# Kernel tuning notes

Measured on AMD Instinct MI355X. Metric: run time of the kernel, lower is better.

The kernel has to match this reference:

```python
import jax, jax.numpy as jnp
import numpy as np

NEG = -1e9  # matches torch masked_fill value (additive, not -inf)

def setup_inputs() -> dict:
    key = jax.random.key(0)
    k1, k2, k3, k4 = jax.random.split(key, 4)
    B, H, S, D = 8, 16, 1024, 64
    q = jax.random.normal(k1, (B, H, S, D), dtype=jnp.float32)
    k = jax.random.normal(k2, (B, H, S, D), dtype=jnp.float32)
    v = jax.random.normal(k3, (B, H, S, D), dtype=jnp.float32)
    event_length = jax.random.randint(k4, (B,), 0, S, dtype=jnp.int32)
    return {"q": q, "k": k, "v": v, "event_length": event_length}

def reference(q, k, v, event_length):
    B, H, S, D = q.shape
    scale = 1.0 / jnp.sqrt(jnp.asarray(D, dtype=q.dtype))
    idx = jnp.arange(S)
    # valid[b, i] = i < event_length[b]
    valid = idx[None, :] < event_length[:, None]            # [B, S]
    # additive mask: 0 where (row valid AND col valid), else -1e9
    pair = valid[:, :, None] & valid[:, None, :]            # [B, S, S]
    attn_mask = jnp.where(pair, 0.0, NEG).astype(q.dtype)[:, None, :, :]  # [B,1,S,S]
    scores = jnp.einsum('bhqd,bhkd->bhqk', q, k) * scale + attn_mask
    probs = jax.nn.softmax(scores, axis=-1)
    out = jnp.einsum('bhqk,bhkd->bhqd', probs, v)
    return out
```

## Files before the change

### kernel.cpp

```cpp
#include <hip/hip_runtime.h>


#define Sdim 1024
#define Ddim 64
#define PITCH 72

typedef float f32x4 __attribute__((ext_vector_type(4)));
typedef _Float16 f16x8 __attribute__((ext_vector_type(8)));
typedef unsigned short u16x8 __attribute__((ext_vector_type(8)));
typedef unsigned int u32x2 __attribute__((ext_vector_type(2)));

union FragU { u16x8 u; f16x8 h; };

__device__ __forceinline__ unsigned pk2(float a, float b) {
  auto h = __builtin_amdgcn_cvt_pkrtz(a, b);
  return __builtin_bit_cast(unsigned, h);
}

__device__ __forceinline__ float fexp2(float x) {
  float r;
  asm("v_exp_f32 %0, %1" : "=v"(r) : "v"(x));
  return r;
}

__global__ __launch_bounds__(256, 3)
void attn_fwd(const float* __restrict__ Q, const float* __restrict__ K,
              const float* __restrict__ V, const int* __restrict__ EL,
              float* __restrict__ Out, unsigned* __restrict__ queues) {
  __shared__ unsigned short k_lds[64 * PITCH];
  __shared__ unsigned short v_lds[64 * PITCH];
  __shared__ unsigned short p_lds[4][32 * PITCH];
  __shared__ int s_item;

  const int tid   = threadIdx.x;
  const int homeq = blockIdx.x & 7;
  unsigned* ctr = &queues[homeq * 32];

  const int w    = tid >> 6;
  const int lane = tid & 63;
  const int r    = lane & 15;
  const int hi   = lane >> 4;
  const int r3   = r >> 3;
  const int sr   = tid >> 4;
  const int sc   = tid & 15;
  const int vskew = ((sc >> 1) & 7) * 8;

  for (;;) {
    __syncthreads();
    if (tid == 0) s_item = (int)atomicAdd(ctr, 1u);
    __syncthreads();
    const int g = s_item;
    if (g >= 128) break;

    const int pan = g >> 3;
    const int qt  = g & 7;
    const int bh  = pan * 8 + homeq;
    const int L   = EL[bh >> 4];

    const size_t base = (size_t)bh * Sdim * Ddim;
    const float* Qb = Q + base;
    const float* Kb = K + base;
    const float* Vb = V + base;
    float* ob = Out + base;

    const int q0blk = qt * 128;

    if (q0blk >= L) {
      float* red = (float*)k_lds;
      const int sc4 = sc * 4;
      const float* vp = Vb + (size_t)sr * Ddim + sc4;
      float4 acc = {0.f, 0.f, 0.f, 0.f};
#pragma unroll 8
      for (int i = 0; i < 64; ++i) {
        float4 a = *(const float4*)(vp + (size_t)i * 16 * Ddim);
        acc.x += a.x; acc.y += a.y; acc.z += a.z; acc.w += a.w;
      }
      *(float4*)&red[sr * 68 + sc4] = acc;
      __syncthreads();
      if (tid < 16) {
        float4 s = {0.f, 0.f, 0.f, 0.f};
#pragma unroll
        for (int i = 0; i < 16; ++i) {
          float4 a = *(const float4*)&red[i * 68 + tid * 4];
          s.x += a.x; s.y += a.y; s.z += a.z; s.w += a.w;
        }
        const float inv = 1.0f / 1024.0f;
        s.x *= inv; s.y *= inv; s.z *= inv; s.w *= inv;
        *(float4*)&red[16 * 68 + tid * 4] = s;
      }
      __syncthreads();
      const float4 cm = *(const float4*)&red[16 * 68 + sc4];
#pragma unroll
      for (int pp = 0; pp < 8; ++pp) {
        int row = q0blk + pp * 16 + sr;
        *(float4*)&ob[(size_t)row * Ddim + sc4] = cm;
      }
      continue;
    }

    const int q0w      = q0blk + w * 32;
    const bool wValid  = q0w < L;
    const bool wAllVal = (q0w + 32) <= L;
    const int kFull    = (L + 63) >> 6;
    const int ktB      = L >> 6;
    const bool straddle = (q0blk + 128) > L;

    const bool qv0 = (q0w + r) < L;
    const bool qv1 = (q0w + 16 + r) < L;

    const float SCL = 0.125f * 1.44269504088896340736f;
    f16x8 qf[2][2];
    if (wValid) {
#pragma unroll
      for (int qc = 0; qc < 2; ++qc)
#pragma unroll
        for (int kk = 0; kk < 2; ++kk) {
          const float* pq = Qb + (size_t)(q0w + qc * 16 + r) * Ddim + kk * 32 + hi * 8;
          float4 a = *(const float4*)pq;
          float4 cc = *(const float4*)(pq + 4);
          union { unsigned u[4]; f16x8 hh; } f;
          f.u[0] = pk2(a.x * SCL, a.y * SCL);   f.u[1] = pk2(a.z * SCL, a.w * SCL);
          f.u[2] = pk2(cc.x * SCL, cc.y * SCL); f.u[3] = pk2(cc.z * SCL, cc.w * SCL);
          qf[qc][kk] = f.hh;
        }
    }

    const f32x4 zero4 = {0.f, 0.f, 0.f, 0.f};
    f32x4 oacc[2][4];
#pragma unroll
    for (int qc = 0; qc < 2; ++qc)
#pragma unroll
      for (int dc = 0; dc < 4; ++dc) oacc[qc][dc] = zero4;

    float lpart[2] = {0.f, 0.f};

    const float* pK = Kb + (size_t)sr * Ddim + sc * 4;
    const float* pV = Vb + (size_t)(sr * 4) * Ddim + sc * 4;

    float4 kpre[4], vpre[4];
    auto LOADK = [&](int k0_) {
#pragma unroll
      for (int i = 0; i < 4; ++i)
        kpre[i] = *(const float4*)(pK + (size_t)(k0_ + 16 * i) * Ddim);
    };
    auto LOADV = [&](int k0_) {
#pragma unroll
      for (int jj = 0; jj < 4; ++jj)
        vpre[jj] = *(const float4*)(pV + (size_t)(k0_ + jj) * Ddim);
    };

    LOADK(0);
    LOADV(0);

    for (int kt = 0; kt < kFull; ++kt) {
      const int k0 = kt * 64;
      __syncthreads();

#pragma unroll
      for (int i = 0; i < 4; ++i) {
        u32x2 o;
        o[0] = pk2(kpre[i].x, kpre[i].y); o[1] = pk2(kpre[i].z, kpre[i].w);
        *(u32x2*)&k_lds[(16 * i + sr) * PITCH + sc * 4] = o;
      }
      {
        const int cp = (sr * 4 + vskew) & 63;
        u32x2 o;
        o[0] = pk2(vpre[0].x, vpre[1].x); o[1] = pk2(vpre[2].x, vpre[3].x);
        *(u32x2*)&v_lds[(sc * 4 + 0) * PITCH + cp] = o;
        o[0] = pk2(vpre[0].y, vpre[1].y); o[1] = pk2(vpre[2].y, vpre[3].y);
        *(u32x2*)&v_lds[(sc * 4 + 1) * PITCH + cp] = o;
        o[0] = pk2(vpre[0].z, vpre[1].z); o[1] = pk2(vpre[2].z, vpre[3].z);
        *(u32x2*)&v_lds[(sc * 4 + 2) * PITCH + cp] = o;
        o[0] = pk2(vpre[0].w, vpre[1].w); o[1] = pk2(vpre[2].w, vpre[3].w);
        *(u32x2*)&v_lds[(sc * 4 + 3) * PITCH + cp] = o;
      }
      __syncthreads();

      if (kt + 1 < kFull) { LOADK(k0 + 64); LOADV(k0 + 64); }

      if (wValid) {
        f32x4 sacc[2][4];
#pragma unroll
        for (int qc = 0; qc < 2; ++qc)
#pragma unroll
          for (int kc = 0; kc < 4; ++kc) sacc[qc][kc] = zero4;

        __builtin_amdgcn_s_setprio(1);
#pragma unroll
        for (int kc = 0; kc < 4; ++kc)
#pragma unroll
          for (int kk = 0; kk < 2; ++kk) {
            FragU kf;
            kf.u = *(const u16x8*)&k_lds[(kc * 16 + r) * PITCH + kk * 32 + hi * 8];
            sacc[0][kc] = __builtin_amdgcn_mfma_f32_16x16x32_f16(kf.h, qf[0][kk], sacc[0][kc], 0, 0, 0);
            sacc[1][kc] = __builtin_amdgcn_mfma_f32_16x16x32_f16(kf.h, qf[1][kk], sacc[1][kc], 0, 0, 0);
          }
        __builtin_amdgcn_s_setprio(0);

        const bool noMask = wAllVal && (kt != ktB);
#pragma unroll
        for (int qc = 0; qc < 2; ++qc) {
          const bool qv = qc ? qv1 : qv0;
          float ls = 0.f;
#pragma unroll
          for (int kc = 0; kc < 4; ++kc) {
            float pr[4];
#pragma unroll
            for (int rg = 0; rg < 4; ++rg) {
              float s = sacc[qc][kc][rg];
              if (!noMask) {
                int kg = k0 + kc * 16 + 4 * hi + rg;
                s = (qv && kg < L) ? s : -__builtin_inff();
              }
              pr[rg] = fexp2(s);
              ls += pr[rg];
            }
            u32x2 o;
            o[0] = pk2(pr[0], pr[1]);
            o[1] = pk2(pr[2], pr[3]);
            *(u32x2*)&p_lds[w][(qc * 16 + r) * PITCH + kc * 16 + 4 * hi] = o;
          }
          lpart[qc] += ls;
        }

        asm volatile("s_waitcnt lgkmcnt(0)" ::: "memory");
        __builtin_amdgcn_sched_barrier(0);

        __builtin_amdgcn_s_setprio(1);
#pragma unroll
        for (int ks = 0; ks < 2; ++ks) {
          FragU pf0, pf1;
          pf0.u = *(const u16x8*)&p_lds[w][(0  + r) * PITCH + ks * 32 + hi * 8];
          pf1.u = *(const u16x8*)&p_lds[w][(16 + r) * PITCH + ks * 32 + hi * 8];
#pragma unroll
          for (int dc = 0; dc < 4; ++dc) {
            const int vcp = (ks * 32 + hi * 8 + (((dc * 2 + r3) & 7) << 3)) & 63;
            FragU vf;
            vf.u = *(const u16x8*)&v_lds[(dc * 16 + r) * PITCH + vcp];
            oacc[0][dc] = __builtin_amdgcn_mfma_f32_16x16x32_f16(pf0.h, vf.h, oacc[0][dc], 0, 0, 0);
            oacc[1][dc] = __builtin_amdgcn_mfma_f32_16x16x32_f16(pf1.h, vf.h, oacc[1][dc], 0, 0, 0);
          }
        }
        __builtin_amdgcn_s_setprio(0);
      }
    }

#pragma unroll
    for (int qc = 0; qc < 2; ++qc) {
      float l = lpart[qc];
      l += __shfl_xor(l, 16, 64);
      l += __shfl_xor(l, 32, 64);
#pragma unroll
      for (int rg = 0; rg < 4; ++rg) {
        float lsq = __shfl(l, 4 * hi + rg, 64);
        float inv = 1.0f / lsq;
        int qrow = q0w + qc * 16 + 4 * hi + rg;
        if (qrow < L) {
#pragma unroll
          for (int dc = 0; dc < 4; ++dc)
            ob[(size_t)qrow * Ddim + dc * 16 + r] = oacc[qc][dc][rg] * inv;
        }
      }
    }

    if (straddle) {
      __syncthreads();
      float* red = (float*)k_lds;
      const int sc4 = sc * 4;
      const float* vp = Vb + (size_t)sr * Ddim + sc4;
      float4 acc = {0.f, 0.f, 0.f, 0.f};
#pragma unroll 8
      for (int i = 0; i < 64; ++i) {
        float4 a = *(const float4*)(vp + (size_t)i * 16 * Ddim);
        acc.x += a.x; acc.y += a.y; acc.z += a.z; acc.w += a.w;
      }
      *(float4*)&red[sr * 68 + sc4] = acc;
      __syncthreads();
      if (tid < 16) {
        float4 s = {0.f, 0.f, 0.f, 0.f};
#pragma unroll
        for (int i = 0; i < 16; ++i) {
          float4 a = *(const float4*)&red[i * 68 + tid * 4];
          s.x += a.x; s.y += a.y; s.z += a.z; s.w += a.w;
        }
        const float inv = 1.0f / 1024.0f;
        s.x *= inv; s.y *= inv; s.z *= inv; s.w *= inv;
        *(float4*)&red[16 * 68 + tid * 4] = s;
      }
      __syncthreads();
      const float4 cm = *(const float4*)&red[16 * 68 + sc4];
#pragma unroll
      for (int pp = 0; pp < 8; ++pp) {
        int row = q0blk + pp * 16 + sr;
        if (row >= L)
          *(float4*)&ob[(size_t)row * Ddim + sc4] = cm;
      }
    }
  }
}

extern "C" void kernel_launch(void* const* d_in, const int* in_sizes, int n_in,
                              void* d_out, int out_size, void* d_ws, size_t ws_size,
                              hipStream_t stream) {
  const float* q  = (const float*)d_in[0];
  const float* k  = (const float*)d_in[1];
  const float* v  = (const float*)d_in[2];
  const int*   el = (const int*)d_in[3];
  float* out = (float*)d_out;
  hipMemsetAsync(d_ws, 0, 1024, stream);
  dim3 grid(768);
  dim3 block(256);
  hipLaunchKernelGGL(attn_fwd, grid, block, 0, stream, q, k, v, el, out,
                     (unsigned*)d_ws);
}
```

Baseline: 48.41 us.

## Keep P in registers via transposed PV MFMA and stage output through LDS

Removes the per-wave P staging buffer in LDS. The PV product is now computed transposed with 16x16x16 f16 MFMAs, so the exp'd probabilities feed straight from registers as the B operand, with V fragments read as 4-wide slices. The epilogue writes normalized output through an LDS scratch so each lane stores full float4 rows, and the grid grows from 768 to 1024 blocks now that LDS use is smaller and more blocks can be resident. The trade-off is twice as many smaller MFMAs, an extra __syncthreads, and a round trip through LDS in the epilogue.

```diff
diff --git a/kernel.cpp b/kernel.cpp
--- a/kernel.cpp
+++ b/kernel.cpp
@@ -7,10 +7,12 @@
 
 typedef float f32x4 __attribute__((ext_vector_type(4)));
 typedef _Float16 f16x8 __attribute__((ext_vector_type(8)));
+typedef _Float16 f16x4 __attribute__((ext_vector_type(4)));
 typedef unsigned short u16x8 __attribute__((ext_vector_type(8)));
 typedef unsigned int u32x2 __attribute__((ext_vector_type(2)));
 
 union FragU { u16x8 u; f16x8 h; };
+union Frag4 { u32x2 u; f16x4 h; };
 
 __device__ __forceinline__ unsigned pk2(float a, float b) {
   auto h = __builtin_amdgcn_cvt_pkrtz(a, b);
@@ -27,10 +29,10 @@
 void attn_fwd(const float* __restrict__ Q, const float* __restrict__ K,
               const float* __restrict__ V, const int* __restrict__ EL,
               float* __restrict__ Out, unsigned* __restrict__ queues) {
-  __shared__ unsigned short k_lds[64 * PITCH];
-  __shared__ unsigned short v_lds[64 * PITCH];
-  __shared__ unsigned short p_lds[4][32 * PITCH];
+  __shared__ unsigned short lds_all[2 * 64 * PITCH];
   __shared__ int s_item;
+  unsigned short* k_lds = lds_all;
+  unsigned short* v_lds = lds_all + 64 * PITCH;
 
   const int tid   = threadIdx.x;
   const int homeq = blockIdx.x & 7;
@@ -66,7 +68,7 @@
     const int q0blk = qt * 128;
 
     if (q0blk >= L) {
-      float* red = (float*)k_lds;
+      float* red = (float*)lds_all;
       const int sc4 = sc * 4;
       const float* vp = Vb + (size_t)sr * Ddim + sc4;
       float4 acc = {0.f, 0.f, 0.f, 0.f};
@@ -126,11 +128,11 @@
     }
 
     const f32x4 zero4 = {0.f, 0.f, 0.f, 0.f};
-    f32x4 oacc[2][4];
+    f32x4 otacc[2][4];
 #pragma unroll
     for (int qc = 0; qc < 2; ++qc)
 #pragma unroll
-      for (int dc = 0; dc < 4; ++dc) oacc[qc][dc] = zero4;
+      for (int dc = 0; dc < 4; ++dc) otacc[qc][dc] = zero4;
 
     float lpart[2] = {0.f, 0.f};
 
@@ -198,6 +200,7 @@
         __builtin_amdgcn_s_setprio(0);
 
         const bool noMask = wAllVal && (kt != ktB);
+        Frag4 pf[2][4];
 #pragma unroll
         for (int qc = 0; qc < 2; ++qc) {
           const bool qv = qc ? qv1 : qv0;
@@ -215,57 +218,62 @@
               pr[rg] = fexp2(s);
               ls += pr[rg];
             }
-            u32x2 o;
-            o[0] = pk2(pr[0], pr[1]);
-            o[1] = pk2(pr[2], pr[3]);
-            *(u32x2*)&p_lds[w][(qc * 16 + r) * PITCH + kc * 16 + 4 * hi] = o;
+            pf[qc][kc].u[0] = pk2(pr[0], pr[1]);
+            pf[qc][kc].u[1] = pk2(pr[2], pr[3]);
           }
           lpart[qc] += ls;
         }
 
-        asm volatile("s_waitcnt lgkmcnt(0)" ::: "memory");
-        __builtin_amdgcn_sched_barrier(0);
-
         __builtin_amdgcn_s_setprio(1);
 #pragma unroll
-        for (int ks = 0; ks < 2; ++ks) {
-          FragU pf0, pf1;
-          pf0.u = *(const u16x8*)&p_lds[w][(0  + r) * PITCH + ks * 32 + hi * 8];
-          pf1.u = *(const u16x8*)&p_lds[w][(16 + r) * PITCH + ks * 32 + hi * 8];
+        for (int kc = 0; kc < 4; ++kc)
 #pragma unroll
           for (int dc = 0; dc < 4; ++dc) {
-            const int vcp = (ks * 32 + hi * 8 + (((dc * 2 + r3) & 7) << 3)) & 63;
-            FragU vf;
-            vf.u = *(const u16x8*)&v_lds[(dc * 16 + r) * PITCH + vcp];
-            oacc[0][dc] = __builtin_amdgcn_mfma_f32_16x16x32_f16(pf0.h, vf.h, oacc[0][dc], 0, 0, 0);
-            oacc[1][dc] = __builtin_amdgcn_mfma_f32_16x16x32_f16(pf1.h, vf.h, oacc[1][dc], 0, 0, 0);
+            const int col = (kc * 16 + 4 * hi + (((2 * dc + r3) & 7) << 3)) & 63;
+            Frag4 vf;
+            vf.u = *(const u32x2*)&v_lds[(dc * 16 + r) * PITCH + col];
+            otacc[0][dc] = __builtin_amdgcn_mfma_f32_16x16x16f16(vf.h, pf[0][kc].h, otacc[0][dc], 0, 0, 0);
+            otacc[1][dc] = __builtin_amdgcn_mfma_f32_16x16x16f16(vf.h, pf[1][kc].h, otacc[1][dc], 0, 0, 0);
           }
-        }
         __builtin_amdgcn_s_setprio(0);
       }
     }
 
+    __syncthreads();
+    float* scr = (float*)lds_all + w * (16 * 68);
 #pragma unroll
     for (int qc = 0; qc < 2; ++qc) {
       float l = lpart[qc];
       l += __shfl_xor(l, 16, 64);
       l += __shfl_xor(l, 32, 64);
-#pragma unroll
-      for (int rg = 0; rg < 4; ++rg) {
-        float lsq = __shfl(l, 4 * hi + rg, 64);
-        float inv = 1.0f / lsq;
-        int qrow = q0w + qc * 16 + 4 * hi + rg;
-        if (qrow < L) {
-#pragma unroll
-          for (int dc = 0; dc < 4; ++dc)
-            ob[(size_t)qrow * Ddim + dc * 16 + r] = oacc[qc][dc][rg] * inv;
-        }
-      }
+      const float inv = 1.0f / l;
+      if (wValid) {
+#pragma unroll
+        for (int dc = 0; dc < 4; ++dc)
+#pragma unroll
+          for (int rg = 0; rg < 4; ++rg)
+            scr[r * 68 + dc * 16 + 4 * hi + rg] = otacc[qc][dc][rg] * inv;
+      }
+      asm volatile("s_waitcnt lgkmcnt(0)" ::: "memory");
+      __builtin_amdgcn_sched_barrier(0);
+      if (wValid) {
+        const int rowq = lane >> 2, cs = lane & 3;
+        const int q = q0w + qc * 16 + rowq;
+        if (q < L) {
+#pragma unroll
+          for (int i = 0; i < 4; ++i) {
+            float4 vv = *(const float4*)&scr[rowq * 68 + cs * 16 + i * 4];
+            *(float4*)&ob[(size_t)q * Ddim + cs * 16 + i * 4] = vv;
+          }
+        }
+      }
+      asm volatile("s_waitcnt lgkmcnt(0)" ::: "memory");
+      __builtin_amdgcn_sched_barrier(0);
     }
 
     if (straddle) {
       __syncthreads();
-      float* red = (float*)k_lds;
+      float* red = (float*)lds_all;
       const int sc4 = sc * 4;
       const float* vp = Vb + (size_t)sr * Ddim + sc4;
       float4 acc = {0.f, 0.f, 0.f, 0.f};
@@ -308,7 +316,7 @@
   const int*   el = (const int*)d_in[3];
   float* out = (float*)d_out;
   hipMemsetAsync(d_ws, 0, 1024, stream);
-  dim3 grid(768);
+  dim3 grid(1024);
   dim3 block(256);
   hipLaunchKernelGGL(attn_fwd, grid, block, 0, stream, q, k, v, el, out,
                      (unsigned*)d_ws);
```

New measurement: 49.31 us. No clear change (+1.9%).
